# Performance work log

Hardware: AMD Instinct MI355X
Metric: run time of the kernel (lower is better)

Reference implementation:

```python
import jax, jax.numpy as jnp
import numpy as np

DIM = 512
B = 16
L = 2048
MLP_RATIO = 4
GATE_HID = max(DIM // 4, 8)  # 128
EPS = 1e-5


def _ln(x, g, b):
    mu = jnp.mean(x, axis=-1, keepdims=True)
    var = jnp.mean(jnp.square(x - mu), axis=-1, keepdims=True)
    return (x - mu) * jax.lax.rsqrt(var + EPS) * g + b


def _dwconv(h, w, b, pad):
    # h: [B, C, L], w: [C, 1, k] depthwise
    y = jax.lax.conv_general_dilated(
        h, w, window_strides=(1,), padding=[(pad, pad)],
        dimension_numbers=('NCH', 'OIH', 'NCH'), feature_group_count=h.shape[1])
    return y + b[None, :, None]


def setup_inputs() -> dict:
    key = jax.random.key(0)
    ks = jax.random.split(key, 16)
    d = DIM
    hid = d * MLP_RATIO
    s = lambda k, shape, scale: jax.random.normal(k, shape, dtype=jnp.float32) * scale
    return {
        'x': jax.random.normal(ks[0], (B, L, d), dtype=jnp.float32),
        'ln1_g': jnp.ones((d,), jnp.float32), 'ln1_b': jnp.zeros((d,), jnp.float32),
        'w3': s(ks[1], (d, 1, 3), 0.3), 'b3': jnp.zeros((d,), jnp.float32),
        'w5': s(ks[2], (d, 1, 5), 0.3), 'b5': jnp.zeros((d,), jnp.float32),
        'w7': s(ks[3], (d, 1, 7), 0.3), 'b7': jnp.zeros((d,), jnp.float32),
        'wmix': s(ks[4], (d, d), 0.03), 'bmix': jnp.zeros((d,), jnp.float32),
        'cg_w1': s(ks[5], (d, GATE_HID), 0.03), 'cg_b1': jnp.zeros((GATE_HID,), jnp.float32),
        'cg_w2': s(ks[6], (GATE_HID, d), 0.05), 'cg_b2': jnp.zeros((d,), jnp.float32),
        'wout': s(ks[7], (d, d), 0.03), 'bout': jnp.zeros((d,), jnp.float32),
        'ls1': jnp.full((d,), 1e-4, jnp.float32),
        'ln2_g': jnp.ones((d,), jnp.float32), 'ln2_b': jnp.zeros((d,), jnp.float32),
        'ffn_w1': s(ks[8], (d, hid), 0.03), 'ffn_b1': jnp.zeros((hid,), jnp.float32),
        'ffn_w2': s(ks[9], (hid, d), 0.02), 'ffn_b2': jnp.zeros((d,), jnp.float32),
        'ls2': jnp.full((d,), 1e-4, jnp.float32),
    }


def reference(x, ln1_g, ln1_b, w3, b3, w5, b5, w7, b7, wmix, bmix,
              cg_w1, cg_b1, cg_w2, cg_b2, wout, bout, ls1,
              ln2_g, ln2_b, ffn_w1, ffn_b1, ffn_w2, ffn_b2, ls2):
    gelu = lambda v: jax.nn.gelu(v, approximate=False)
    # norm + transpose to channels-first [B, D, L]
    h = jnp.transpose(_ln(x, ln1_g, ln1_b), (0, 2, 1))
    mixed = (_dwconv(h, w3, b3, 1) + _dwconv(h, w5, b5, 2) + _dwconv(h, w7, b7, 3)) / 3.0
    # 1x1 conv == per-position channel GEMM
    mixed = jnp.einsum('bcl,co->bol', gelu(mixed), wmix.T) + bmix[None, :, None]
    channel_token = jnp.mean(mixed, axis=-1)  # [B, D]
    gate = jax.nn.sigmoid(gelu(channel_token @ cg_w1 + cg_b1) @ cg_w2 + cg_b2)  # [B, D]
    attn_like = jnp.transpose(mixed * gate[:, :, None], (0, 2, 1))  # [B, L, D]
    x = x + (attn_like @ wout + bout) * ls1  # dropout is identity in eval
    h2 = _ln(x, ln2_g, ln2_b)
    x = x + (gelu(h2 @ ffn_w1 + ffn_b1) @ ffn_w2 + ffn_b2) * ls2
    return x
```

## Files before the change

kernel.cpp:

```cpp
#include <hip/hip_runtime.h>
#include <hip/hip_bf16.h>
#include <stdint.h>
#include <math.h>

#define DIMC 512
#define SEQ  2048
#define NB   16
#define MTOT (NB * SEQ)
#define HID  2048

#define SWZ(row) ((((row) & 7) << 4) | ((row) & 8))

typedef float v4f __attribute__((ext_vector_type(4)));

__device__ __forceinline__ float bf2f(unsigned short u) {
  union { unsigned int i; float f; } v; v.i = ((unsigned int)u) << 16; return v.f;
}
__device__ __forceinline__ unsigned short f2bf(float f) {
  union { float f; unsigned int i; } v; v.f = f;
  unsigned int r = v.i + 0x7fffu + ((v.i >> 16) & 1u);
  return (unsigned short)(r >> 16);
}
__device__ __forceinline__ float gelu_f(float v) {
  return 0.5f * v * (1.f + erff(v * 0.70710678118654752440f));
}
__device__ __forceinline__ float gelu_fast(float v) {
  float e = __expf(v * -1.702f);
  return v * __builtin_amdgcn_rcpf(1.f + e);
}
__device__ __forceinline__ unsigned short pk_fp8(float a, float b) {
  return (unsigned short)__builtin_amdgcn_cvt_pk_fp8_f32(a, b, 0, false);
}
__device__ __forceinline__ unsigned int pk_fp8x4(float a, float b, float c, float d) {
  int lo = __builtin_amdgcn_cvt_pk_fp8_f32(a, b, 0, false);
  return (unsigned int)__builtin_amdgcn_cvt_pk_fp8_f32(c, d, lo, true);
}

typedef __attribute__((address_space(1))) const void cglobal_void;
typedef __attribute__((address_space(3))) void lds_void;
__device__ __forceinline__ void load16_lds(const void* g, void* l) {
  __builtin_amdgcn_global_load_lds((cglobal_void*)g, (lds_void*)l, 16, 0, 0);
}

__global__ __launch_bounds__(256) void pack_all(
    const float* __restrict__ wmix, const float* __restrict__ wout,
    const float* __restrict__ ffn_w1, const float* __restrict__ ffn_w2,
    unsigned char* __restrict__ wmix8, unsigned char* __restrict__ wout8,
    unsigned char* __restrict__ w18, unsigned char* __restrict__ w28,
    float* __restrict__ gsum) {
  int p = blockIdx.x * 256 + threadIdx.x;
  if (p < NB * DIMC) gsum[p] = 0.f;

  const float* in; unsigned char* out; int R, C, trans;
  if (p < 131072)      { in = wmix;   out = wmix8; R = 512;  C = 512;  trans = 0; }
  else if (p < 262144) { in = wout;   out = wout8; R = 512;  C = 512;  trans = 1; p -= 131072; }
  else if (p < 786432) { in = ffn_w1; out = w18;   R = 2048; C = 512;  trans = 1; p -= 262144; }
  else                 { in = ffn_w2; out = w28;   R = 512;  C = 2048; trans = 1; p -= 786432; }
  int r = (p * 2) / C, c = (p * 2) - r * C;
  float v0, v1;
  if (trans) { v0 = in[(size_t)c * R + r]; v1 = in[(size_t)(c + 1) * R + r]; }
  else       { v0 = in[(size_t)r * C + c]; v1 = in[(size_t)r * C + c + 1]; }
  *(unsigned short*)(out + (size_t)r * C + (c ^ SWZ(r))) = pk_fp8(v0, v1);
}

__global__ __launch_bounds__(256) void ln1_conv(
    const float* __restrict__ x, const float* __restrict__ lg, const float* __restrict__ lb,
    const float* __restrict__ w3, const float* __restrict__ b3,
    const float* __restrict__ w5, const float* __restrict__ b5,
    const float* __restrict__ w7, const float* __restrict__ b7,
    unsigned char* __restrict__ gout, float* __restrict__ gsum) {
  __shared__ __align__(16) unsigned short ht[38 * DIMC];
  int blk = blockIdx.x;
  int b = blk >> 6;
  int l0 = (blk & 63) << 5;
  int tid = threadIdx.x, lane = tid & 63, w = tid >> 6;

  for (int r = w; r < 38; r += 4) {
    int l = l0 - 3 + r;
    unsigned short* hrow = ht + r * DIMC;
    if (l < 0 || l >= SEQ) {
      ushort4 z; z.x = z.y = z.z = z.w = 0;
      *(ushort4*)&hrow[lane * 4] = z;
      *(ushort4*)&hrow[256 + lane * 4] = z;
    } else {
      const float4* xp = (const float4*)(x + ((size_t)(b * SEQ + l)) * DIMC);
      float4 v0 = xp[lane], v1 = xp[lane + 64];
      float s = v0.x + v0.y + v0.z + v0.w + v1.x + v1.y + v1.z + v1.w;
      float q = v0.x * v0.x + v0.y * v0.y + v0.z * v0.z + v0.w * v0.w +
                v1.x * v1.x + v1.y * v1.y + v1.z * v1.z + v1.w * v1.w;
#pragma unroll
      for (int o = 32; o > 0; o >>= 1) { s += __shfl_xor(s, o); q += __shfl_xor(q, o); }
      float mu = s * (1.f / 512.f);
      float rs = rsqrtf(q * (1.f / 512.f) - mu * mu + 1e-5f);
      float4 ga = ((const float4*)lg)[lane], gb = ((const float4*)lg)[lane + 64];
      float4 ba = ((const float4*)lb)[lane], bb = ((const float4*)lb)[lane + 64];
      ushort4 o0, o1;
      o0.x = f2bf((v0.x - mu) * rs * ga.x + ba.x);
      o0.y = f2bf((v0.y - mu) * rs * ga.y + ba.y);
      o0.z = f2bf((v0.z - mu) * rs * ga.z + ba.z);
      o0.w = f2bf((v0.w - mu) * rs * ga.w + ba.w);
      o1.x = f2bf((v1.x - mu) * rs * gb.x + bb.x);
      o1.y = f2bf((v1.y - mu) * rs * gb.y + bb.y);
      o1.z = f2bf((v1.z - mu) * rs * gb.z + bb.z);
      o1.w = f2bf((v1.w - mu) * rs * gb.w + bb.w);
      *(ushort4*)&hrow[lane * 4] = o0;
      *(ushort4*)&hrow[256 + lane * 4] = o1;
    }
  }
  __syncthreads();

  int d0 = tid << 1;
  float t3[2][3], t5[2][5], t7[2][7], cb[2];
#pragma unroll
  for (int j = 0; j < 2; j++) {
    int d = d0 + j;
    cb[j] = b3[d] + b5[d] + b7[d];
#pragma unroll
    for (int t = 0; t < 3; t++) t3[j][t] = w3[d * 3 + t];
#pragma unroll
    for (int t = 0; t < 5; t++) t5[j][t] = w5[d * 5 + t];
#pragma unroll
    for (int t = 0; t < 7; t++) t7[j][t] = w7[d * 7 + t];
  }
  float sum0 = 0.f, sum1 = 0.f;
  size_t rbase = ((size_t)(b * SEQ + l0)) * DIMC;
  for (int l = 0; l < 32; l++) {
    float h0[7], h1[7];
#pragma unroll
    for (int r = 0; r < 7; r++) {
      unsigned int pk = *(const unsigned int*)&ht[(l + r) * DIMC + d0];
      h0[r] = bf2f((unsigned short)pk);
      h1[r] = bf2f((unsigned short)(pk >> 16));
    }
    float a0 = cb[0], a1 = cb[1];
#pragma unroll
    for (int t = 0; t < 7; t++) { a0 += t7[0][t] * h0[t];     a1 += t7[1][t] * h1[t]; }
#pragma unroll
    for (int t = 0; t < 5; t++) { a0 += t5[0][t] * h0[t + 1]; a1 += t5[1][t] * h1[t + 1]; }
#pragma unroll
    for (int t = 0; t < 3; t++) { a0 += t3[0][t] * h0[t + 2]; a1 += t3[1][t] * h1[t + 2]; }
    a0 *= (1.f / 3.f); a1 *= (1.f / 3.f);
    float g0 = gelu_fast(a0), g1 = gelu_fast(a1);
    *(unsigned short*)(gout + rbase + (size_t)l * DIMC + (d0 ^ SWZ(l))) = pk_fp8(g0, g1);
    sum0 += g0; sum1 += g1;
  }
  atomicAdd(&gsum[b * DIMC + d0], sum0);
  atomicAdd(&gsum[b * DIMC + d0 + 1], sum1);
}

__global__ __launch_bounds__(1024) void gate_kernel(
    const float* __restrict__ gsum, const float* __restrict__ wmix, const float* __restrict__ bmix,
    const float* __restrict__ cg_w1, const float* __restrict__ cg_b1,
    const float* __restrict__ cg_w2, const float* __restrict__ cg_b2,
    float* __restrict__ gate) {
  __shared__ float gbar[512];
  __shared__ float ct[512];
  __shared__ float part2[8][128];
  __shared__ float t1[128];
  __shared__ float part3[2][512];
  int b = blockIdx.x, tid = threadIdx.x;
  int lane = tid & 63, w = tid >> 6;

  if (tid < 512) gbar[tid] = gsum[b * 512 + tid] * (1.f / (float)SEQ);
  __syncthreads();

  {
    const float4* gb4 = (const float4*)gbar;
    float4 g0 = gb4[lane * 2], g1 = gb4[lane * 2 + 1];
#pragma unroll 4
    for (int i = 0; i < 32; i++) {
      int o = w * 32 + i;
      const float4* wr = (const float4*)(wmix + (size_t)o * 512);
      float4 a0 = wr[lane * 2], a1 = wr[lane * 2 + 1];
      float s = a0.x * g0.x + a0.y * g0.y + a0.z * g0.z + a0.w * g0.w +
                a1.x * g1.x + a1.y * g1.y + a1.z * g1.z + a1.w * g1.w;
#pragma unroll
      for (int off = 32; off > 0; off >>= 1) s += __shfl_xor(s, off);
      if (lane == 0) ct[o] = s + bmix[o];
    }
  }
  __syncthreads();

  {
    int h = tid & 127, g = tid >> 7;
    float s = 0.f;
    const float* wp = cg_w1 + (size_t)(g * 64) * 128 + h;
#pragma unroll 8
    for (int c = 0; c < 64; c++) s += ct[g * 64 + c] * wp[c * 128];
    part2[g][h] = s;
  }
  __syncthreads();
  if (tid < 128) {
    float s = cg_b1[tid];
#pragma unroll
    for (int g = 0; g < 8; g++) s += part2[g][tid];
    t1[tid] = gelu_f(s);
  }
  __syncthreads();

  {
    int o = tid & 511, g = tid >> 9;
    float s = 0.f;
    const float* wp = cg_w2 + (size_t)(g * 64) * 512 + o;
#pragma unroll 8
    for (int h = 0; h < 64; h++) s += t1[g * 64 + h] * wp[h * 512];
    part3[g][o] = s;
  }
  __syncthreads();
  if (tid < 512) {
    float s = cg_b2[tid] + part3[0][tid] + part3[1][tid];
    gate[b * 512 + tid] = 1.f / (1.f + expf(-s));
  }
}

__global__ __launch_bounds__(256) void ln2_kernel(
    const float* __restrict__ y, const float* __restrict__ lg, const float* __restrict__ lb,
    unsigned char* __restrict__ h2) {
  int tok = (blockIdx.x << 2) + (threadIdx.x >> 6);
  int lane = threadIdx.x & 63;
  const float4* yp = (const float4*)(y + ((size_t)tok) * DIMC);
  float4 v0 = yp[lane], v1 = yp[lane + 64];
  float s = v0.x + v0.y + v0.z + v0.w + v1.x + v1.y + v1.z + v1.w;
  float q = v0.x * v0.x + v0.y * v0.y + v0.z * v0.z + v0.w * v0.w +
            v1.x * v1.x + v1.y * v1.y + v1.z * v1.z + v1.w * v1.w;
#pragma unroll
  for (int o = 32; o > 0; o >>= 1) { s += __shfl_xor(s, o); q += __shfl_xor(q, o); }
  float mu = s * (1.f / 512.f);
  float rs = rsqrtf(q * (1.f / 512.f) - mu * mu + 1e-5f);
  float4 ga = ((const float4*)lg)[lane], gb = ((const float4*)lg)[lane + 64];
  float4 ba = ((const float4*)lb)[lane], bb = ((const float4*)lb)[lane + 64];
  unsigned char* hp = h2 + (size_t)tok * DIMC;
  int sw = SWZ(tok);
  *(unsigned int*)(hp + ((lane * 4) ^ sw)) = pk_fp8x4(
      (v0.x - mu) * rs * ga.x + ba.x, (v0.y - mu) * rs * ga.y + ba.y,
      (v0.z - mu) * rs * ga.z + ba.z, (v0.w - mu) * rs * ga.w + ba.w);
  *(unsigned int*)(hp + (256 + ((lane * 4) ^ sw))) = pk_fp8x4(
      (v1.x - mu) * rs * gb.x + bb.x, (v1.y - mu) * rs * gb.y + bb.y,
      (v1.z - mu) * rs * gb.z + bb.z, (v1.w - mu) * rs * gb.w + bb.w);
}

template <int MODE>
__global__ __launch_bounds__(256) void gemm_bt(
    const unsigned char* __restrict__ A, int lda,
    const unsigned char* __restrict__ B, int ldb,
    const float* __restrict__ bias, const float* __restrict__ scale,
    const float* __restrict__ resid, void* __restrict__ outp,
    int N, int K, const float* __restrict__ gate) {
  __shared__ __align__(16) unsigned char smem[32768];
  unsigned char* As = smem;
  unsigned char* Bs = smem + 16384;
  float* ebuf = (float*)smem;

  const int m0 = blockIdx.x * 128, n0 = blockIdx.y * 128;
  const int tid = threadIdx.x, lane = tid & 63, w = tid >> 6;
  const int wm = w >> 1, wn = w & 1, quad = lane >> 4, cn = lane & 15;
  const int srow = lane >> 3;
  const int scol = (lane & 7) << 4;
  const int rswz = SWZ(cn);

  v4f acc[4][4];
  v4f zero4 = {0.f, 0.f, 0.f, 0.f};
#pragma unroll
  for (int i = 0; i < 4; i++)
#pragma unroll
    for (int j = 0; j < 4; j++) acc[i][j] = zero4;

  for (int k0 = 0; k0 < K; k0 += 128) {
    __syncthreads();
#pragma unroll
    for (int s = 0; s < 4; s++) {
      int seg = (w << 2) + s;
      int row = (seg << 3) + srow;
      load16_lds(A + (size_t)(m0 + row) * lda + k0 + scol, &As[seg * 1024]);
      load16_lds(B + (size_t)(n0 + row) * ldb + k0 + scol, &Bs[seg * 1024]);
    }
    __syncthreads();
#pragma unroll
    for (int kk = 0; kk < 4; kk++) {
      long af[4], bf[4];
      int pcol = ((kk << 5) + (quad << 3)) ^ rswz;
#pragma unroll
      for (int mt = 0; mt < 4; mt++)
        af[mt] = *(const long*)&As[(wm * 64 + mt * 16 + cn) * 128 + pcol];
#pragma unroll
      for (int nt = 0; nt < 4; nt++)
        bf[nt] = *(const long*)&Bs[(wn * 64 + nt * 16 + cn) * 128 + pcol];
#pragma unroll
      for (int mt = 0; mt < 4; mt++)
#pragma unroll
        for (int nt = 0; nt < 4; nt++)
          acc[mt][nt] = __builtin_amdgcn_mfma_f32_16x16x32_fp8_fp8(af[mt], bf[nt], acc[mt][nt], 0, 0, 0);
    }
  }

  const int bb = (MODE == 1) ? (m0 >> 11) : 0;
#pragma unroll
  for (int h = 0; h < 2; h++) {
    __syncthreads();
    if (wm == h) {
      const int exsw = (quad & 1) << 4;
#pragma unroll
      for (int mt = 0; mt < 4; mt++)
#pragma unroll
        for (int nt = 0; nt < 4; nt++)
#pragma unroll
          for (int r = 0; r < 4; r++)
            ebuf[(mt * 16 + quad * 4 + r) * 128 + ((wn * 64 + nt * 16 + cn) ^ exsw)] = acc[mt][nt][r];
    }
    __syncthreads();
#pragma unroll
    for (int i = 0; i < 8; i++) {
      int fi = (i << 8) + tid;
      int r = fi >> 5, c4 = fi & 31;
      int row = m0 + (h << 6) + r;
      int col = n0 + (c4 << 2);
      const float* e = &ebuf[(fi << 2) ^ ((r & 4) << 2)];
      float v0 = e[0], v1 = e[1], v2 = e[2], v3 = e[3];
      float4 bv = *(const float4*)&bias[col];
      v0 += bv.x; v1 += bv.y; v2 += bv.z; v3 += bv.w;
      size_t idx = (size_t)row * N + col;
      size_t sidx = (size_t)row * N + (col ^ SWZ(row));
      if (MODE == 1) {
        float4 gv = *(const float4*)&gate[bb * 512 + col];
        *(unsigned int*)((unsigned char*)outp + sidx) =
            pk_fp8x4(v0 * gv.x, v1 * gv.y, v2 * gv.z, v3 * gv.w);
      } else if (MODE == 2) {
        float4 sv = *(const float4*)&scale[col];
        float4 rv = *(const float4*)&resid[idx];
        float4 o; o.x = rv.x + v0 * sv.x; o.y = rv.y + v1 * sv.y;
        o.z = rv.z + v2 * sv.z; o.w = rv.w + v3 * sv.w;
        *(float4*)((float*)outp + idx) = o;
      } else if (MODE == 3) {
        *(unsigned int*)((unsigned char*)outp + sidx) =
            pk_fp8x4(gelu_fast(v0), gelu_fast(v1), gelu_fast(v2), gelu_fast(v3));
      } else {
        float4 sv = *(const float4*)&scale[col];
        float* op = (float*)outp + idx;
        float4 ov = *(float4*)op;
        float4 o; o.x = ov.x + v0 * sv.x; o.y = ov.y + v1 * sv.y;
        o.z = ov.z + v2 * sv.z; o.w = ov.w + v3 * sv.w;
        *(float4*)op = o;
      }
    }
  }
}

extern "C" void kernel_launch(void* const* d_in, const int* in_sizes, int n_in,
                              void* d_out, int out_size, void* d_ws, size_t ws_size,
                              hipStream_t stream) {
  (void)in_sizes; (void)n_in; (void)out_size; (void)ws_size;
  const float* x     = (const float*)d_in[0];
  const float* ln1_g = (const float*)d_in[1];
  const float* ln1_b = (const float*)d_in[2];
  const float* w3    = (const float*)d_in[3];
  const float* b3    = (const float*)d_in[4];
  const float* w5    = (const float*)d_in[5];
  const float* b5    = (const float*)d_in[6];
  const float* w7    = (const float*)d_in[7];
  const float* b7    = (const float*)d_in[8];
  const float* wmix  = (const float*)d_in[9];
  const float* bmix  = (const float*)d_in[10];
  const float* cg_w1 = (const float*)d_in[11];
  const float* cg_b1 = (const float*)d_in[12];
  const float* cg_w2 = (const float*)d_in[13];
  const float* cg_b2 = (const float*)d_in[14];
  const float* wout  = (const float*)d_in[15];
  const float* bout  = (const float*)d_in[16];
  const float* ls1   = (const float*)d_in[17];
  const float* ln2_g = (const float*)d_in[18];
  const float* ln2_b = (const float*)d_in[19];
  const float* ffn_w1= (const float*)d_in[20];
  const float* ffn_b1= (const float*)d_in[21];
  const float* ffn_w2= (const float*)d_in[22];
  const float* ffn_b2= (const float*)d_in[23];
  const float* ls2   = (const float*)d_in[24];

  char* ws = (char*)d_ws;
  unsigned char* wmix8 = (unsigned char*)(ws + 0);
  unsigned char* wout8 = (unsigned char*)(ws + 262144);
  unsigned char* w18   = (unsigned char*)(ws + 524288);
  unsigned char* w28   = (unsigned char*)(ws + 1572864);
  float*         gsum  = (float*)(ws + 2621440);
  float*         gate  = (float*)(ws + 2654208);
  unsigned char* gbuf  = (unsigned char*)(ws + 3145728);
  unsigned char* attn  = (unsigned char*)(ws + 19922944);
  unsigned char* h2buf = (unsigned char*)(ws + 36700160);
  unsigned char* tbuf  = gbuf;

  pack_all<<<1310720 / 256, 256, 0, stream>>>(wmix, wout, ffn_w1, ffn_w2,
                                              wmix8, wout8, w18, w28, gsum);

  ln1_conv<<<NB * 64, 256, 0, stream>>>(x, ln1_g, ln1_b, w3, b3, w5, b5, w7, b7, gbuf, gsum);
  gate_kernel<<<NB, 1024, 0, stream>>>(gsum, wmix, bmix, cg_w1, cg_b1, cg_w2, cg_b2, gate);

  dim3 grid_d(MTOT / 128, DIMC / 128);
  gemm_bt<1><<<grid_d, 256, 0, stream>>>(gbuf, 512, wmix8, 512,
                                         bmix, nullptr, nullptr, attn, 512, 512, gate);
  gemm_bt<2><<<grid_d, 256, 0, stream>>>(attn, 512, wout8, 512,
                                         bout, ls1, x, d_out, 512, 512, nullptr);
  ln2_kernel<<<MTOT / 4, 256, 0, stream>>>((const float*)d_out, ln2_g, ln2_b, h2buf);

  const int MC = 16384;
  for (int c = 0; c < 2; c++) {
    size_t r0 = (size_t)c * MC;
    dim3 g3(MC / 128, HID / 128);
    gemm_bt<3><<<g3, 256, 0, stream>>>(h2buf + r0 * 512, 512, w18, 512,
                                       ffn_b1, nullptr, nullptr, tbuf, HID, 512, nullptr);
    dim3 g4(MC / 128, DIMC / 128);
    gemm_bt<4><<<g4, 256, 0, stream>>>(tbuf, 2048, w28, 2048,
                                       ffn_b2, ls2, nullptr,
                                       (float*)d_out + r0 * 512, 512, 2048, nullptr);
  }
}
```

Measured before the change: 436.9 us.

## Remap GEMM blocks per XCD and fold weight packing into ln1_conv

The GEMM grid becomes one-dimensional and each block's tile is remapped so that blocks landing on the same XCD (round-robin by block id mod 8) cover a contiguous range of M rows and all N tiles. Those blocks then share the A rows in that XCD's L2. The separate pack_all kernel is removed: its weight transposition and FP8 packing now runs at the start of ln1_conv, and gsum is zeroed with hipMemsetAsync. This saves one kernel launch, but adds strided transposed weight reads to ln1_conv ahead of its main work.

```diff
diff --git a/kernel.cpp b/kernel.cpp
--- a/kernel.cpp
+++ b/kernel.cpp
@@ -42,38 +42,36 @@
   __builtin_amdgcn_global_load_lds((cglobal_void*)g, (lds_void*)l, 16, 0, 0);
 }
 
-__global__ __launch_bounds__(256) void pack_all(
-    const float* __restrict__ wmix, const float* __restrict__ wout,
-    const float* __restrict__ ffn_w1, const float* __restrict__ ffn_w2,
-    unsigned char* __restrict__ wmix8, unsigned char* __restrict__ wout8,
-    unsigned char* __restrict__ w18, unsigned char* __restrict__ w28,
-    float* __restrict__ gsum) {
-  int p = blockIdx.x * 256 + threadIdx.x;
-  if (p < NB * DIMC) gsum[p] = 0.f;
-
-  const float* in; unsigned char* out; int R, C, trans;
-  if (p < 131072)      { in = wmix;   out = wmix8; R = 512;  C = 512;  trans = 0; }
-  else if (p < 262144) { in = wout;   out = wout8; R = 512;  C = 512;  trans = 1; p -= 131072; }
-  else if (p < 786432) { in = ffn_w1; out = w18;   R = 2048; C = 512;  trans = 1; p -= 262144; }
-  else                 { in = ffn_w2; out = w28;   R = 512;  C = 2048; trans = 1; p -= 786432; }
-  int r = (p * 2) / C, c = (p * 2) - r * C;
-  float v0, v1;
-  if (trans) { v0 = in[(size_t)c * R + r]; v1 = in[(size_t)(c + 1) * R + r]; }
-  else       { v0 = in[(size_t)r * C + c]; v1 = in[(size_t)r * C + c + 1]; }
-  *(unsigned short*)(out + (size_t)r * C + (c ^ SWZ(r))) = pk_fp8(v0, v1);
-}
-
 __global__ __launch_bounds__(256) void ln1_conv(
     const float* __restrict__ x, const float* __restrict__ lg, const float* __restrict__ lb,
     const float* __restrict__ w3, const float* __restrict__ b3,
     const float* __restrict__ w5, const float* __restrict__ b5,
     const float* __restrict__ w7, const float* __restrict__ b7,
+    const float* __restrict__ wmix, const float* __restrict__ wout,
+    const float* __restrict__ ffn_w1, const float* __restrict__ ffn_w2,
+    unsigned char* __restrict__ wmix8, unsigned char* __restrict__ wout8,
+    unsigned char* __restrict__ w18, unsigned char* __restrict__ w28,
     unsigned char* __restrict__ gout, float* __restrict__ gsum) {
   __shared__ __align__(16) unsigned short ht[38 * DIMC];
   int blk = blockIdx.x;
   int b = blk >> 6;
   int l0 = (blk & 63) << 5;
   int tid = threadIdx.x, lane = tid & 63, w = tid >> 6;
+
+#pragma unroll
+  for (int j = 0; j < 5; j++) {
+    int p = j * 262144 + blk * 256 + tid;
+    const float* in; unsigned char* out; int R, C, trans;
+    if (p < 131072)      { in = wmix;   out = wmix8; R = 512;  C = 512;  trans = 0; }
+    else if (p < 262144) { in = wout;   out = wout8; R = 512;  C = 512;  trans = 1; p -= 131072; }
+    else if (p < 786432) { in = ffn_w1; out = w18;   R = 2048; C = 512;  trans = 1; p -= 262144; }
+    else                 { in = ffn_w2; out = w28;   R = 512;  C = 2048; trans = 1; p -= 786432; }
+    int r = (p * 2) / C, c = (p * 2) - r * C;
+    float v0, v1;
+    if (trans) { v0 = in[(size_t)c * R + r]; v1 = in[(size_t)(c + 1) * R + r]; }
+    else       { v0 = in[(size_t)r * C + c]; v1 = in[(size_t)r * C + c + 1]; }
+    *(unsigned short*)(out + (size_t)r * C + (c ^ SWZ(r))) = pk_fp8(v0, v1);
+  }
 
   for (int r = w; r < 38; r += 4) {
     int l = l0 - 3 + r;
@@ -251,7 +249,13 @@
   unsigned char* Bs = smem + 16384;
   float* ebuf = (float*)smem;
 
-  const int m0 = blockIdx.x * 128, n0 = blockIdx.y * 128;
+  const int gy = N >> 7;
+  const int h0 = blockIdx.x;
+  const int xcd = h0 & 7, slot = h0 >> 3;
+  const int gxp = (int)(gridDim.x >> 3) / gy;
+  const int xl = slot / gy, yl = slot - xl * gy;
+  const int m0 = (xcd * gxp + xl) << 7, n0 = yl << 7;
+
   const int tid = threadIdx.x, lane = tid & 63, w = tid >> 6;
   const int wm = w >> 1, wn = w & 1, quad = lane >> 4, cn = lane & 15;
   const int srow = lane >> 3;
@@ -295,9 +299,9 @@
 
   const int bb = (MODE == 1) ? (m0 >> 11) : 0;
 #pragma unroll
-  for (int h = 0; h < 2; h++) {
+  for (int hh = 0; hh < 2; hh++) {
     __syncthreads();
-    if (wm == h) {
+    if (wm == hh) {
       const int exsw = (quad & 1) << 4;
 #pragma unroll
       for (int mt = 0; mt < 4; mt++)
@@ -312,7 +316,7 @@
     for (int i = 0; i < 8; i++) {
       int fi = (i << 8) + tid;
       int r = fi >> 5, c4 = fi & 31;
-      int row = m0 + (h << 6) + r;
+      int row = m0 + (hh << 6) + r;
       int col = n0 + (c4 << 2);
       const float* e = &ebuf[(fi << 2) ^ ((r & 4) << 2)];
       float v0 = e[0], v1 = e[1], v2 = e[2], v3 = e[3];
@@ -387,28 +391,26 @@
   unsigned char* h2buf = (unsigned char*)(ws + 36700160);
   unsigned char* tbuf  = gbuf;
 
-  pack_all<<<1310720 / 256, 256, 0, stream>>>(wmix, wout, ffn_w1, ffn_w2,
-                                              wmix8, wout8, w18, w28, gsum);
-
-  ln1_conv<<<NB * 64, 256, 0, stream>>>(x, ln1_g, ln1_b, w3, b3, w5, b5, w7, b7, gbuf, gsum);
+  hipMemsetAsync(gsum, 0, NB * DIMC * sizeof(float), stream);
+
+  ln1_conv<<<NB * 64, 256, 0, stream>>>(x, ln1_g, ln1_b, w3, b3, w5, b5, w7, b7,
+                                        wmix, wout, ffn_w1, ffn_w2,
+                                        wmix8, wout8, w18, w28, gbuf, gsum);
   gate_kernel<<<NB, 1024, 0, stream>>>(gsum, wmix, bmix, cg_w1, cg_b1, cg_w2, cg_b2, gate);
 
-  dim3 grid_d(MTOT / 128, DIMC / 128);
-  gemm_bt<1><<<grid_d, 256, 0, stream>>>(gbuf, 512, wmix8, 512,
-                                         bmix, nullptr, nullptr, attn, 512, 512, gate);
-  gemm_bt<2><<<grid_d, 256, 0, stream>>>(attn, 512, wout8, 512,
-                                         bout, ls1, x, d_out, 512, 512, nullptr);
+  gemm_bt<1><<<(MTOT / 128) * (DIMC / 128), 256, 0, stream>>>(
+      gbuf, 512, wmix8, 512, bmix, nullptr, nullptr, attn, 512, 512, gate);
+  gemm_bt<2><<<(MTOT / 128) * (DIMC / 128), 256, 0, stream>>>(
+      attn, 512, wout8, 512, bout, ls1, x, d_out, 512, 512, nullptr);
   ln2_kernel<<<MTOT / 4, 256, 0, stream>>>((const float*)d_out, ln2_g, ln2_b, h2buf);
 
   const int MC = 16384;
   for (int c = 0; c < 2; c++) {
     size_t r0 = (size_t)c * MC;
-    dim3 g3(MC / 128, HID / 128);
-    gemm_bt<3><<<g3, 256, 0, stream>>>(h2buf + r0 * 512, 512, w18, 512,
-                                       ffn_b1, nullptr, nullptr, tbuf, HID, 512, nullptr);
-    dim3 g4(MC / 128, DIMC / 128);
-    gemm_bt<4><<<g4, 256, 0, stream>>>(tbuf, 2048, w28, 2048,
-                                       ffn_b2, ls2, nullptr,
-                                       (float*)d_out + r0 * 512, 512, 2048, nullptr);
-  }
-}
+    gemm_bt<3><<<(MC / 128) * (HID / 128), 256, 0, stream>>>(
+        h2buf + r0 * 512, 512, w18, 512, ffn_b1, nullptr, nullptr, tbuf, HID, 512, nullptr);
+    gemm_bt<4><<<(MC / 128) * (DIMC / 128), 256, 0, stream>>>(
+        tbuf, 2048, w28, 2048, ffn_b2, ls2, nullptr,
+        (float*)d_out + r0 * 512, 512, 2048, nullptr);
+  }
+}
```

Measured after the change: 438.0 us. No clear change (+0.3%).
